# Kernel optimization log

Hardware: AMD Instinct MI355X
Metric: run time of the kernel (lower is better)

## Reference

```python
import jax, jax.numpy as jnp
import numpy as np

B, S, D, H = 4, 1024, 1024, 16
HD = D // H
EPS = 1e-5


def _layernorm(x, g, b):
    m = jnp.mean(x, axis=-1, keepdims=True)
    v = jnp.mean((x - m) ** 2, axis=-1, keepdims=True)
    return (x - m) * jax.lax.rsqrt(v + EPS) * g + b


def setup_inputs() -> dict:
    key = jax.random.key(0)
    ks = jax.random.split(key, 8)
    sc = 1.0 / np.sqrt(D)
    return {
        "x": jax.random.normal(ks[0], (B, S, D), dtype=jnp.float32),
        "seq_len": jax.random.randint(ks[1], (B,), 1, S + 1, dtype=jnp.int32),
        "Wq": jax.random.normal(ks[2], (D, D), dtype=jnp.float32) * sc,
        "bq": jnp.zeros((D,), dtype=jnp.float32),
        "Wk": jax.random.normal(ks[3], (D, D), dtype=jnp.float32) * sc,
        "bk": jnp.zeros((D,), dtype=jnp.float32),
        "Wv": jax.random.normal(ks[4], (D, D), dtype=jnp.float32) * sc,
        "bv": jnp.zeros((D,), dtype=jnp.float32),
        "ln_g": jnp.ones((HD,), dtype=jnp.float32),
        "ln_b": jnp.zeros((HD,), dtype=jnp.float32),
    }


def reference(x, seq_len, Wq, bq, Wk, bk, Wv, bv, ln_g, ln_b):
    # Faithful quirk: k and v are projections of the ALREADY projected q.
    q = x @ Wq.T + bq                      # [B,S,D]
    k = q @ Wk.T + bk
    v = q @ Wv.T + bv
    # [B,S,D] -> [B,H,S,HD]
    def split_heads(t):
        return t.reshape(B, S, H, HD).transpose(0, 2, 1, 3)
    q, k, v = split_heads(q), split_heads(k), split_heads(v)
    # shared per-head LayerNorm over head_dim
    q = _layernorm(q, ln_g, ln_b)
    k = _layernorm(k, ln_g, ln_b)
    v = _layernorm(v, ln_g, ln_b)
    # raw scores (no temperature scaling in the original; temperature=1.0 unused)
    scores = jnp.einsum("bhqd,bhkd->bhqk", q, k)
    # encoder_mask: multiplicative validity mask on key positions, repeated per head
    mask = (jnp.arange(S)[None, :] < seq_len[:, None]).astype(scores.dtype)  # [B,S]
    scores = scores * mask[:, None, None, :]
    attn = jax.nn.softmax(scores, axis=-1)
    # dropout is identity at inference
    out = jnp.einsum("bhqk,bhkd->bhqd", attn, v)
    return out.transpose(0, 2, 1, 3).reshape(B, S, D)
```

## Files before the change

### kernel.cpp

```cpp
#include <hip/hip_runtime.h>

#define B_  4
#define S_  1024
#define D_  1024
#define H_  16
#define HD_ 64
#define EPS_ 1e-5f

typedef _Float16 f16x8 __attribute__((ext_vector_type(8)));
typedef _Float16 f16x4 __attribute__((ext_vector_type(4)));
typedef __bf16 bf16x8 __attribute__((ext_vector_type(8)));
typedef float  f32x4  __attribute__((ext_vector_type(4)));
typedef unsigned short ushort4v __attribute__((ext_vector_type(4)));
typedef unsigned short ushort8v __attribute__((ext_vector_type(8)));

#define GLD16(gp, lp) __builtin_amdgcn_global_load_lds( \
    (const __attribute__((address_space(1))) void*)(gp), \
    (__attribute__((address_space(3))) void*)(lp), 16, 0, 0)

__global__ __launch_bounds__(256) void cvt_all(
    const float* __restrict__ x,  _Float16* __restrict__ xh,
    const float* __restrict__ Wq, _Float16* __restrict__ wqh,
    const float* __restrict__ Wk, _Float16* __restrict__ wkh,
    const float* __restrict__ Wv, _Float16* __restrict__ wvh,
    float* __restrict__ Vtail) {
  int bid = blockIdx.x;
  if (bid >= 7168) {
    int i = (bid - 7168) * 1024 + threadIdx.x * 4;
    *(float4*)(Vtail + i) = make_float4(0.f, 0.f, 0.f, 0.f);
    return;
  }
  const float* src; _Float16* dst; int base;
  if (bid < 4096)      { src = x;  dst = xh;  base = bid; }
  else if (bid < 5120) { src = Wq; dst = wqh; base = bid - 4096; }
  else if (bid < 6144) { src = Wk; dst = wkh; base = bid - 5120; }
  else                 { src = Wv; dst = wvh; base = bid - 6144; }
  int i = base * 1024 + threadIdx.x * 4;
  float4 f = *(const float4*)(src + i);
  f16x4 h;
  h.x = (_Float16)f.x; h.y = (_Float16)f.y; h.z = (_Float16)f.z; h.w = (_Float16)f.w;
  *(f16x4*)(dst + i) = h;
}

__global__ __launch_bounds__(256, 2) void gemm_q_ln(
    const _Float16* __restrict__ A,
    const _Float16* __restrict__ Bw,
    const float* __restrict__ bias,
    const float* __restrict__ ln_g, const float* __restrict__ ln_b,
    _Float16* __restrict__ qh,
    _Float16* __restrict__ Qn)
{
  __shared__ _Float16 As[2 * 128 * 32];
  __shared__ _Float16 Bs[2 * 64 * 32];

  int tid  = threadIdx.x;
  int lane = tid & 63;
  int wave = tid >> 6;
  int qd = lane >> 4, l15 = lane & 15;

  long row0 = (long)blockIdx.y * 128;
  long col0 = (long)blockIdx.x * 64;

  int r_a = tid >> 2;
  int c_a = (tid & 3) * 8;

  f32x4 acc[2][4] = {};

  for (int kk = 0; kk < D_; kk += 64) {
    GLD16(A  + (row0 + r_a) * D_ + kk + c_a,           As + tid * 8);
    GLD16(A  + (row0 + 64 + r_a) * D_ + kk + c_a,      As + 2048 + tid * 8);
    GLD16(A  + (row0 + r_a) * D_ + kk + 32 + c_a,      As + 4096 + tid * 8);
    GLD16(A  + (row0 + 64 + r_a) * D_ + kk + 32 + c_a, As + 6144 + tid * 8);
    GLD16(Bw + (col0 + r_a) * D_ + kk + c_a,           Bs + tid * 8);
    GLD16(Bw + (col0 + r_a) * D_ + kk + 32 + c_a,      Bs + 2048 + tid * 8);
    __syncthreads();

    for (int ks = 0; ks < 2; ks++) {
      f16x8 af[2], bfr[4];
      for (int i = 0; i < 2; i++)
        af[i]  = *(const f16x8*)(As + ks * 4096 + (wave * 32 + i * 16 + l15) * 32 + qd * 8);
      for (int j = 0; j < 4; j++)
        bfr[j] = *(const f16x8*)(Bs + ks * 2048 + (j * 16 + l15) * 32 + qd * 8);
      for (int i = 0; i < 2; i++)
        for (int j = 0; j < 4; j++)
          acc[i][j] = __builtin_amdgcn_mfma_f32_16x16x32_f16(af[i], bfr[j], acc[i][j], 0, 0, 0);
    }
    __syncthreads();
  }

  int h = blockIdx.x;
  long rw = row0 + wave * 32;
  int bb = (int)(rw >> 10);
  long bh = (long)bb * H_ + h;
  float gv[4], bl[4], bc[4];
  for (int j = 0; j < 4; j++) {
    int d = j * 16 + l15;
    gv[j] = ln_g[d]; bl[j] = ln_b[d]; bc[j] = bias[h * 64 + d];
  }
  for (int i = 0; i < 2; i++) {
    float m4[4], i4[4];
    for (int r = 0; r < 4; r++) {
      float s = 0.f, q = 0.f;
      for (int j = 0; j < 4; j++) {
        float y = acc[i][j][r] + bc[j];
        s += y; q = fmaf(y, y, q);
      }
      for (int off = 1; off < 16; off <<= 1) {
        s += __shfl_xor(s, off, 64);
        q += __shfl_xor(q, off, 64);
      }
      float m = s * (1.f / 64.f);
      m4[r] = m;
      i4[r] = rsqrtf(q * (1.f / 64.f) - m * m + EPS_);
    }
    for (int r = 0; r < 4; r++) {
      long srow = rw + i * 16 + qd * 4 + r;
      long sloc = srow & (S_ - 1);
      for (int j = 0; j < 4; j++) {
        float y = acc[i][j][r] + bc[j];
        qh[srow * D_ + h * 64 + j * 16 + l15] = (_Float16)y;
        Qn[(bh * S_ + sloc) * HD_ + j * 16 + l15] =
            (_Float16)((y - m4[r]) * i4[r] * gv[j] + bl[j]);
      }
    }
  }
}

__global__ __launch_bounds__(256, 2) void gemm_kv_ln(
    const _Float16* __restrict__ A,
    const _Float16* __restrict__ Bk, const float* __restrict__ bk,
    const _Float16* __restrict__ Bv, const float* __restrict__ bv,
    const float* __restrict__ ln_g, const float* __restrict__ ln_b,
    const int* __restrict__ seq_len,
    _Float16* __restrict__ Kn,
    unsigned short* __restrict__ Vt,
    float* __restrict__ Vtail)
{
  const _Float16* Bm = blockIdx.z ? Bv : Bk;
  const float* bias  = blockIdx.z ? bv : bk;

  __shared__ _Float16 As[2 * 128 * 32];
  __shared__ _Float16 Bs[2 * 128 * 32];

  int tid  = threadIdx.x;
  int lane = tid & 63;
  int wave = tid >> 6;
  int wm = wave >> 1, wn = wave & 1;
  int qd = lane >> 4, l15 = lane & 15;

  long row0 = (long)blockIdx.y * 128;
  long col0 = (long)blockIdx.x * 128;

  int r_a = tid >> 2;
  int c_a = (tid & 3) * 8;

  f32x4 acc[4][4] = {};

  for (int kk = 0; kk < D_; kk += 64) {
    GLD16(A  + (row0 + r_a) * D_ + kk + c_a,           As + tid * 8);
    GLD16(A  + (row0 + 64 + r_a) * D_ + kk + c_a,      As + 2048 + tid * 8);
    GLD16(A  + (row0 + r_a) * D_ + kk + 32 + c_a,      As + 4096 + tid * 8);
    GLD16(A  + (row0 + 64 + r_a) * D_ + kk + 32 + c_a, As + 6144 + tid * 8);
    GLD16(Bm + (col0 + r_a) * D_ + kk + c_a,           Bs + tid * 8);
    GLD16(Bm + (col0 + 64 + r_a) * D_ + kk + c_a,      Bs + 2048 + tid * 8);
    GLD16(Bm + (col0 + r_a) * D_ + kk + 32 + c_a,      Bs + 4096 + tid * 8);
    GLD16(Bm + (col0 + 64 + r_a) * D_ + kk + 32 + c_a, Bs + 6144 + tid * 8);
    __syncthreads();

    for (int ks = 0; ks < 2; ks++) {
      f16x8 af[4], bfr[4];
      for (int t = 0; t < 4; t++) {
        af[t]  = *(const f16x8*)(As + ks * 4096 + (wm * 64 + t * 16 + l15) * 32 + qd * 8);
        bfr[t] = *(const f16x8*)(Bs + ks * 4096 + (wn * 64 + t * 16 + l15) * 32 + qd * 8);
      }
      for (int i = 0; i < 4; i++)
        for (int j = 0; j < 4; j++)
          acc[i][j] = __builtin_amdgcn_mfma_f32_16x16x32_f16(af[i], bfr[j], acc[i][j], 0, 0, 0);
    }
    __syncthreads();
  }

  int h = blockIdx.x * 2 + wn;
  long rw = row0 + wm * 64;
  int bb = (int)(rw >> 10);
  long bh = (long)bb * H_ + h;
  float gv[4], bl[4], bc[4];
  for (int j = 0; j < 4; j++) {
    int d = j * 16 + l15;
    gv[j] = ln_g[d]; bl[j] = ln_b[d]; bc[j] = bias[h * 64 + d];
  }

  if (blockIdx.z == 0) {
    for (int i = 0; i < 4; i++) {
      float m4[4], i4[4];
      for (int r = 0; r < 4; r++) {
        float s = 0.f, q = 0.f;
        for (int j = 0; j < 4; j++) {
          float y = acc[i][j][r] + bc[j];
          s += y; q = fmaf(y, y, q);
        }
        for (int off = 1; off < 16; off <<= 1) {
          s += __shfl_xor(s, off, 64);
          q += __shfl_xor(q, off, 64);
        }
        float m = s * (1.f / 64.f);
        m4[r] = m;
        i4[r] = rsqrtf(q * (1.f / 64.f) - m * m + EPS_);
      }
      for (int r = 0; r < 4; r++) {
        long sloc = (rw + i * 16 + qd * 4 + r) & (S_ - 1);
        for (int j = 0; j < 4; j++) {
          float y = acc[i][j][r] + bc[j];
          Kn[(bh * S_ + sloc) * HD_ + j * 16 + l15] =
              (_Float16)((y - m4[r]) * i4[r] * gv[j] + bl[j]);
        }
      }
    }
  } else {
    int len = seq_len[bb];
    float tsum[4] = {0.f, 0.f, 0.f, 0.f};
    for (int i = 0; i < 4; i++) {
      float m4[4], i4[4];
      for (int r = 0; r < 4; r++) {
        float s = 0.f, q = 0.f;
        for (int j = 0; j < 4; j++) {
          float y = acc[i][j][r] + bc[j];
          s += y; q = fmaf(y, y, q);
        }
        for (int off = 1; off < 16; off <<= 1) {
          s += __shfl_xor(s, off, 64);
          q += __shfl_xor(q, off, 64);
        }
        float m = s * (1.f / 64.f);
        m4[r] = m;
        i4[r] = rsqrtf(q * (1.f / 64.f) - m * m + EPS_);
      }
      int s0loc = (int)((rw + i * 16 + qd * 4) & (S_ - 1));
      for (int j = 0; j < 4; j++) {
        ushort4v w;
        for (int r = 0; r < 4; r++) {
          float y = acc[i][j][r] + bc[j];
          float vo = (y - m4[r]) * i4[r] * gv[j] + bl[j];
          __bf16 vb = (__bf16)vo;
          union { __bf16 hh; unsigned short uu; } cv; cv.hh = vb;
          w[r] = cv.uu;
          if (s0loc + r >= len) tsum[j] += (float)vb;
        }
        *(ushort4v*)(Vt + (bh * HD_ + j * 16 + l15) * S_ + s0loc) = w;
      }
    }
    if (((int)(rw & (S_ - 1)) + 64) > len)
      for (int j = 0; j < 4; j++)
        atomicAdd(&Vtail[bh * HD_ + j * 16 + l15], tsum[j]);
  }
}

__global__ __launch_bounds__(256, 4) void attn(
    const _Float16* __restrict__ Qn,
    const _Float16* __restrict__ Kn,
    const unsigned short* __restrict__ Vt,
    const float* __restrict__ Vtail,
    const int* __restrict__ seq_len,
    float* __restrict__ out)
{
  __shared__ _Float16 Ks[2][64 * 32];
  __shared__ unsigned short Vts[2][64 * 32];
  __shared__ __bf16 Ps[4][16 * 72];

  int tid = threadIdx.x, lane = tid & 63, wave = tid >> 6;
  int qd = lane >> 4, l15 = lane & 15;
  int b = blockIdx.x;
  int h = blockIdx.y;
  int q0 = blockIdx.z * 64;
  long bh = (long)b * H_ + h;
  int len = seq_len[b];
  int ntile = (len + 63) >> 6;

  int skey = tid >> 2;
  int schunk = (tid & 3) * 8;

  f16x8 qf[2];
  {
    const _Float16* qp = Qn + (bh * S_ + q0 + wave * 16 + l15) * HD_;
    qf[0] = *(const f16x8*)(qp + qd * 8);
    qf[1] = *(const f16x8*)(qp + 32 + qd * 8);
  }
  float tv[4];
  for (int t = 0; t < 4; t++) tv[t] = Vtail[bh * HD_ + t * 16 + l15];

  f32x4 o[4] = {};
  float den[4] = {0.f, 0.f, 0.f, 0.f};

  for (int kt = 0; kt < ntile; kt++) {
    GLD16(Kn + (bh * S_ + kt * 64 + skey) * HD_ + schunk,      &Ks[0][0] + tid * 8);
    GLD16(Kn + (bh * S_ + kt * 64 + skey) * HD_ + 32 + schunk, &Ks[1][0] + tid * 8);
    GLD16(Vt + (bh * HD_ + skey) * S_ + kt * 64 + schunk,      &Vts[0][0] + tid * 8);
    GLD16(Vt + (bh * HD_ + skey) * S_ + kt * 64 + 32 + schunk, &Vts[1][0] + tid * 8);
    __syncthreads();

    f32x4 sacc[4] = {};
    for (int tn = 0; tn < 4; tn++) {
      f16x8 kf0 = *(const f16x8*)(&Ks[0][0] + (tn * 16 + l15) * 32 + qd * 8);
      f16x8 kf1 = *(const f16x8*)(&Ks[1][0] + (tn * 16 + l15) * 32 + qd * 8);
      sacc[tn] = __builtin_amdgcn_mfma_f32_16x16x32_f16(qf[0], kf0, sacc[tn], 0, 0, 0);
      sacc[tn] = __builtin_amdgcn_mfma_f32_16x16x32_f16(qf[1], kf1, sacc[tn], 0, 0, 0);
    }

    if (kt * 64 + 64 <= len) {
      for (int tn = 0; tn < 4; tn++)
        for (int r = 0; r < 4; r++) {
          float p = __expf(sacc[tn][r]);
          __bf16 pb = (__bf16)p;
          den[r] += (float)pb;
          Ps[wave][(qd * 4 + r) * 72 + tn * 16 + l15] = pb;
        }
    } else {
      for (int tn = 0; tn < 4; tn++) {
        int kg = kt * 64 + tn * 16 + l15;
        bool valid = kg < len;
        for (int r = 0; r < 4; r++) {
          float p = valid ? __expf(sacc[tn][r]) : 0.f;
          __bf16 pb = (__bf16)p;
          den[r] += (float)pb;
          Ps[wave][(qd * 4 + r) * 72 + tn * 16 + l15] = pb;
        }
      }
    }

    bf16x8 pf0 = *(const bf16x8*)(&Ps[wave][l15 * 72 + qd * 8]);
    bf16x8 pf1 = *(const bf16x8*)(&Ps[wave][l15 * 72 + 32 + qd * 8]);
    for (int t = 0; t < 4; t++) {
      bf16x8 vf0 = *(const bf16x8*)(&Vts[0][0] + (t * 16 + l15) * 32 + qd * 8);
      bf16x8 vf1 = *(const bf16x8*)(&Vts[1][0] + (t * 16 + l15) * 32 + qd * 8);
      o[t] = __builtin_amdgcn_mfma_f32_16x16x32_bf16(pf0, vf0, o[t], 0, 0, 0);
      o[t] = __builtin_amdgcn_mfma_f32_16x16x32_bf16(pf1, vf1, o[t], 0, 0, 0);
    }
    __syncthreads();
  }

  for (int t = 0; t < 4; t++)
    for (int r = 0; r < 4; r++) o[t][r] += tv[t];

  float tden = (float)(S_ - len);
  for (int r = 0; r < 4; r++) {
    for (int off = 1; off < 16; off <<= 1)
      den[r] += __shfl_xor(den[r], off, 64);
    den[r] += tden;
  }

  for (int t = 0; t < 4; t++)
    for (int r = 0; r < 4; r++) {
      long s = q0 + wave * 16 + qd * 4 + r;
      long dcol = (long)h * HD_ + t * 16 + l15;
      out[((long)b * S_ + s) * D_ + dcol] = o[t][r] / den[r];
    }
}

extern "C" void kernel_launch(void* const* d_in, const int* in_sizes, int n_in,
                              void* d_out, int out_size, void* d_ws, size_t ws_size,
                              hipStream_t stream) {
  const float* x     = (const float*)d_in[0];
  const int*  seq    = (const int*)d_in[1];
  const float* Wq    = (const float*)d_in[2];
  const float* bq    = (const float*)d_in[3];
  const float* Wk    = (const float*)d_in[4];
  const float* bk    = (const float*)d_in[5];
  const float* Wv    = (const float*)d_in[6];
  const float* bv    = (const float*)d_in[7];
  const float* ln_g  = (const float*)d_in[8];
  const float* ln_b  = (const float*)d_in[9];
  float* out = (float*)d_out;

  char* ws = (char*)d_ws;
  _Float16* xh  = (_Float16*)(ws);
  _Float16* wqh = (_Float16*)(ws + (8l  << 20));
  _Float16* wkh = (_Float16*)(ws + (10l << 20));
  _Float16* wvh = (_Float16*)(ws + (12l << 20));
  float*    Vtail = (float*)(ws + (14l << 20));
  _Float16* qh  = (_Float16*)(ws + (16l << 20));
  _Float16* Qn  = (_Float16*)(ws + (40l << 20));
  _Float16* Kn  = (_Float16*)(ws + (48l << 20));
  unsigned short* Vt = (unsigned short*)(ws + (56l << 20));

  cvt_all<<<7172, 256, 0, stream>>>(x, xh, Wq, wqh, Wk, wkh, Wv, wvh, Vtail);

  dim3 g1(D_ / 64, (B_ * S_) / 128);
  gemm_q_ln<<<g1, 256, 0, stream>>>(xh, wqh, bq, ln_g, ln_b, qh, Qn);

  dim3 g2(D_ / 128, (B_ * S_) / 128, 2);
  gemm_kv_ln<<<g2, 256, 0, stream>>>(qh, wkh, bk, wvh, bv, ln_g, ln_b, seq,
                                     Kn, Vt, Vtail);

  dim3 g4(B_, H_, S_ / 64);
  attn<<<g4, 256, 0, stream>>>(Qn, Kn, Vt, Vtail, seq, out);
}
```

Measured before the change: 168.6 us.

## Fold Wq into K/V weights so K and V project directly from x

```diff
diff --git a/kernel.cpp b/kernel.cpp
--- a/kernel.cpp
+++ b/kernel.cpp
@@ -12,7 +12,6 @@
 typedef __bf16 bf16x8 __attribute__((ext_vector_type(8)));
 typedef float  f32x4  __attribute__((ext_vector_type(4)));
 typedef unsigned short ushort4v __attribute__((ext_vector_type(4)));
-typedef unsigned short ushort8v __attribute__((ext_vector_type(8)));
 
 #define GLD16(gp, lp) __builtin_amdgcn_global_load_lds( \
     (const __attribute__((address_space(1))) void*)(gp), \
@@ -23,10 +22,32 @@
     const float* __restrict__ Wq, _Float16* __restrict__ wqh,
     const float* __restrict__ Wk, _Float16* __restrict__ wkh,
     const float* __restrict__ Wv, _Float16* __restrict__ wvh,
+    _Float16* __restrict__ wqT,
     float* __restrict__ Vtail) {
+  __shared__ _Float16 tl[64][72];
   int bid = blockIdx.x;
+  int tid = threadIdx.x;
+  if (bid >= 7172) {
+    int tb = bid - 7172;
+    int r0 = (tb >> 4) * 64, c0 = (tb & 15) * 64;
+    int r = tid >> 2, cq = (tid & 3) * 16;
+    for (int u = 0; u < 16; u += 4) {
+      float4 f = *(const float4*)(Wq + (long)(r0 + r) * D_ + c0 + cq + u);
+      tl[r][cq + u + 0] = (_Float16)f.x;
+      tl[r][cq + u + 1] = (_Float16)f.y;
+      tl[r][cq + u + 2] = (_Float16)f.z;
+      tl[r][cq + u + 3] = (_Float16)f.w;
+    }
+    __syncthreads();
+    f16x8 o0, o1;
+    for (int u = 0; u < 8; u++) o0[u] = tl[cq + u][r];
+    for (int u = 0; u < 8; u++) o1[u] = tl[cq + 8 + u][r];
+    *(f16x8*)(wqT + (long)(c0 + r) * D_ + r0 + cq) = o0;
+    *(f16x8*)(wqT + (long)(c0 + r) * D_ + r0 + cq + 8) = o1;
+    return;
+  }
   if (bid >= 7168) {
-    int i = (bid - 7168) * 1024 + threadIdx.x * 4;
+    int i = (bid - 7168) * 1024 + tid * 4;
     *(float4*)(Vtail + i) = make_float4(0.f, 0.f, 0.f, 0.f);
     return;
   }
@@ -35,32 +56,67 @@
   else if (bid < 5120) { src = Wq; dst = wqh; base = bid - 4096; }
   else if (bid < 6144) { src = Wk; dst = wkh; base = bid - 5120; }
   else                 { src = Wv; dst = wvh; base = bid - 6144; }
-  int i = base * 1024 + threadIdx.x * 4;
+  int i = base * 1024 + tid * 4;
   float4 f = *(const float4*)(src + i);
   f16x4 h;
   h.x = (_Float16)f.x; h.y = (_Float16)f.y; h.z = (_Float16)f.z; h.w = (_Float16)f.w;
   *(f16x4*)(dst + i) = h;
 }
 
-__global__ __launch_bounds__(256, 2) void gemm_q_ln(
-    const _Float16* __restrict__ A,
-    const _Float16* __restrict__ Bw,
-    const float* __restrict__ bias,
+__global__ __launch_bounds__(256, 2) void proj_q_comb(
+    const _Float16* __restrict__ xh,
+    const _Float16* __restrict__ wqh,
+    const _Float16* __restrict__ wkh,
+    const _Float16* __restrict__ wvh,
+    const _Float16* __restrict__ wqT,
+    const float* __restrict__ Wkf, const float* __restrict__ Wvf,
+    const float* __restrict__ bq,  const float* __restrict__ bk,
+    const float* __restrict__ bv,
     const float* __restrict__ ln_g, const float* __restrict__ ln_b,
-    _Float16* __restrict__ qh,
-    _Float16* __restrict__ Qn)
+    _Float16* __restrict__ Qn,
+    _Float16* __restrict__ wkqh, _Float16* __restrict__ wvqh,
+    float* __restrict__ bkc, float* __restrict__ bvc)
 {
   __shared__ _Float16 As[2 * 128 * 32];
   __shared__ _Float16 Bs[2 * 64 * 32];
 
-  int tid  = threadIdx.x;
+  int bid = blockIdx.x;
+  int tid = threadIdx.x;
+
+  if (bid >= 768) {
+    int bb = bid - 768;
+    int rib = tid >> 4, L = tid & 15;
+    int ro = bb * 16 + rib;
+    int z = ro >> 10, oo = ro & 1023;
+    const float* W    = z ? Wvf : Wkf;
+    const float* bsrc = z ? bv  : bk;
+    float* dst        = z ? bvc : bkc;
+    float s = 0.f;
+    for (int t = 0; t < 64; t++)
+      s += W[(long)oo * D_ + t * 16 + L] * bq[t * 16 + L];
+    for (int off = 1; off < 16; off <<= 1)
+      s += __shfl_xor(s, off, 16);
+    if (L == 0) dst[oo] = s + bsrc[oo];
+    return;
+  }
+
+  bool isq = bid < 512;
+  const _Float16 *A, *Bw;
+  _Float16* Cw = nullptr;
+  int bx, by;
+  if (isq) { A = xh; Bw = wqh; bx = bid & 15; by = bid >> 4; }
+  else {
+    int cb = bid - 512;
+    int z = cb >> 7, cc = cb & 127;
+    bx = cc & 15; by = cc >> 4;
+    A = z ? wvh : wkh; Bw = wqT; Cw = z ? wvqh : wkqh;
+  }
+
   int lane = tid & 63;
   int wave = tid >> 6;
   int qd = lane >> 4, l15 = lane & 15;
-
-  long row0 = (long)blockIdx.y * 128;
-  long col0 = (long)blockIdx.x * 64;
-
+  long row0 = (long)by * 128;
+  long col0 = (long)bx * 64;
   int r_a = tid >> 2;
   int c_a = (tid & 3) * 8;
 
@@ -88,6 +144,104 @@
     __syncthreads();
   }
 
+  if (!isq) {
+    for (int i = 0; i < 2; i++)
+      for (int r = 0; r < 4; r++) {
+        long row = row0 + wave * 32 + i * 16 + qd * 4 + r;
+        for (int j = 0; j < 4; j++)
+          Cw[row * D_ + col0 + j * 16 + l15] = (_Float16)acc[i][j][r];
+      }
+    return;
+  }
+
+  int h = bx;
+  long rw = row0 + wave * 32;
+  int bb2 = (int)(rw >> 10);
+  long bh = (long)bb2 * H_ + h;
+  float gv[4], bl[4], bc[4];
+  for (int j = 0; j < 4; j++) {
+    int d = j * 16 + l15;
+    gv[j] = ln_g[d]; bl[j] = ln_b[d]; bc[j] = bq[h * 64 + d];
+  }
+  for (int i = 0; i < 2; i++) {
+    float m4[4], i4[4];
+    for (int r = 0; r < 4; r++) {
+      float s = 0.f, q = 0.f;
+      for (int j = 0; j < 4; j++) {
+        float y = acc[i][j][r] + bc[j];
+        s += y; q = fmaf(y, y, q);
+      }
+      for (int off = 1; off < 16; off <<= 1) {
+        s += __shfl_xor(s, off, 64);
+        q += __shfl_xor(q, off, 64);
+      }
+      float m = s * (1.f / 64.f);
+      m4[r] = m;
+      i4[r] = rsqrtf(q * (1.f / 64.f) - m * m + EPS_);
+    }
+    for (int r = 0; r < 4; r++) {
+      long sloc = (rw + i * 16 + qd * 4 + r) & (S_ - 1);
+      for (int j = 0; j < 4; j++) {
+        float y = acc[i][j][r] + bc[j];
+        Qn[(bh * S_ + sloc) * HD_ + j * 16 + l15] =
+            (_Float16)((y - m4[r]) * i4[r] * gv[j] + bl[j]);
+      }
+    }
+  }
+}
+
+__global__ __launch_bounds__(256, 2) void proj_kv(
+    const _Float16* __restrict__ xh,
+    const _Float16* __restrict__ wkqh, const float* __restrict__ bkc,
+    const _Float16* __restrict__ wvqh, const float* __restrict__ bvc,
+    const float* __restrict__ ln_g, const float* __restrict__ ln_b,
+    const int* __restrict__ seq_len,
+    _Float16* __restrict__ Kn,
+    unsigned short* __restrict__ Vt,
+    float* __restrict__ Vtail)
+{
+  int z = blockIdx.z;
+  const _Float16* Bw = z ? wvqh : wkqh;
+  const float* bias  = z ? bvc : bkc;
+
+  __shared__ _Float16 As[2 * 128 * 32];
+  __shared__ _Float16 Bs[2 * 64 * 32];
+
+  int tid  = threadIdx.x;
+  int lane = tid & 63;
+  int wave = tid >> 6;
+  int qd = lane >> 4, l15 = lane & 15;
+
+  long row0 = (long)blockIdx.y * 128;
+  long col0 = (long)blockIdx.x * 64;
+
+  int r_a = tid >> 2;
+  int c_a = (tid & 3) * 8;
+
+  f32x4 acc[2][4] = {};
+
+  for (int kk = 0; kk < D_; kk += 64) {
+    GLD16(xh + (row0 + r_a) * D_ + kk + c_a,           As + tid * 8);
+    GLD16(xh + (row0 + 64 + r_a) * D_ + kk + c_a,      As + 2048 + tid * 8);
+    GLD16(xh + (row0 + r_a) * D_ + kk + 32 + c_a,      As + 4096 + tid * 8);
+    GLD16(xh + (row0 + 64 + r_a) * D_ + kk + 32 + c_a, As + 6144 + tid * 8);
+    GLD16(Bw + (col0 + r_a) * D_ + kk + c_a,           Bs + tid * 8);
+    GLD16(Bw + (col0 + r_a) * D_ + kk + 32 + c_a,      Bs + 2048 + tid * 8);
+    __syncthreads();
+
+    for (int ks = 0; ks < 2; ks++) {
+      f16x8 af[2], bfr[4];
+      for (int i = 0; i < 2; i++)
+        af[i]  = *(const f16x8*)(As + ks * 4096 + (wave * 32 + i * 16 + l15) * 32 + qd * 8);
+      for (int j = 0; j < 4; j++)
+        bfr[j] = *(const f16x8*)(Bs + ks * 2048 + (j * 16 + l15) * 32 + qd * 8);
+      for (int i = 0; i < 2; i++)
+        for (int j = 0; j < 4; j++)
+          acc[i][j] = __builtin_amdgcn_mfma_f32_16x16x32_f16(af[i], bfr[j], acc[i][j], 0, 0, 0);
+    }
+    __syncthreads();
+  }
+
   int h = blockIdx.x;
   long rw = row0 + wave * 32;
   int bb = (int)(rw >> 10);
@@ -97,101 +251,9 @@
     int d = j * 16 + l15;
     gv[j] = ln_g[d]; bl[j] = ln_b[d]; bc[j] = bias[h * 64 + d];
   }
-  for (int i = 0; i < 2; i++) {
-    float m4[4], i4[4];
-    for (int r = 0; r < 4; r++) {
-      float s = 0.f, q = 0.f;
-      for (int j = 0; j < 4; j++) {
-        float y = acc[i][j][r] + bc[j];
-        s += y; q = fmaf(y, y, q);
-      }
-      for (int off = 1; off < 16; off <<= 1) {
-        s += __shfl_xor(s, off, 64);
-        q += __shfl_xor(q, off, 64);
-      }
-      float m = s * (1.f / 64.f);
-      m4[r] = m;
-      i4[r] = rsqrtf(q * (1.f / 64.f) - m * m + EPS_);
-    }
-    for (int r = 0; r < 4; r++) {
-      long srow = rw + i * 16 + qd * 4 + r;
-      long sloc = srow & (S_ - 1);
-      for (int j = 0; j < 4; j++) {
-        float y = acc[i][j][r] + bc[j];
-        qh[srow * D_ + h * 64 + j * 16 + l15] = (_Float16)y;
-        Qn[(bh * S_ + sloc) * HD_ + j * 16 + l15] =
-            (_Float16)((y - m4[r]) * i4[r] * gv[j] + bl[j]);
-      }
-    }
-  }
-}
-
-__global__ __launch_bounds__(256, 2) void gemm_kv_ln(
-    const _Float16* __restrict__ A,
-    const _Float16* __restrict__ Bk, const float* __restrict__ bk,
-    const _Float16* __restrict__ Bv, const float* __restrict__ bv,
-    const float* __restrict__ ln_g, const float* __restrict__ ln_b,
-    const int* __restrict__ seq_len,
-    _Float16* __restrict__ Kn,
-    unsigned short* __restrict__ Vt,
-    float* __restrict__ Vtail)
-{
-  const _Float16* Bm = blockIdx.z ? Bv : Bk;
-  const float* bias  = blockIdx.z ? bv : bk;
-
-  __shared__ _Float16 As[2 * 128 * 32];
-  __shared__ _Float16 Bs[2 * 128 * 32];
-
-  int tid  = threadIdx.x;
-  int lane = tid & 63;
-  int wave = tid >> 6;
-  int wm = wave >> 1, wn = wave & 1;
-  int qd = lane >> 4, l15 = lane & 15;
-
-  long row0 = (long)blockIdx.y * 128;
-  long col0 = (long)blockIdx.x * 128;
-
-  int r_a = tid >> 2;
-  int c_a = (tid & 3) * 8;
-
-  f32x4 acc[4][4] = {};
-
-  for (int kk = 0; kk < D_; kk += 64) {
-    GLD16(A  + (row0 + r_a) * D_ + kk + c_a,           As + tid * 8);
-    GLD16(A  + (row0 + 64 + r_a) * D_ + kk + c_a,      As + 2048 + tid * 8);
-    GLD16(A  + (row0 + r_a) * D_ + kk + 32 + c_a,      As + 4096 + tid * 8);
-    GLD16(A  + (row0 + 64 + r_a) * D_ + kk + 32 + c_a, As + 6144 + tid * 8);
-    GLD16(Bm + (col0 + r_a) * D_ + kk + c_a,           Bs + tid * 8);
-    GLD16(Bm + (col0 + 64 + r_a) * D_ + kk + c_a,      Bs + 2048 + tid * 8);
-    GLD16(Bm + (col0 + r_a) * D_ + kk + 32 + c_a,      Bs + 4096 + tid * 8);
-    GLD16(Bm + (col0 + 64 + r_a) * D_ + kk + 32 + c_a, Bs + 6144 + tid * 8);
-    __syncthreads();
-
-    for (int ks = 0; ks < 2; ks++) {
-      f16x8 af[4], bfr[4];
-      for (int t = 0; t < 4; t++) {
-        af[t]  = *(const f16x8*)(As + ks * 4096 + (wm * 64 + t * 16 + l15) * 32 + qd * 8);
-        bfr[t] = *(const f16x8*)(Bs + ks * 4096 + (wn * 64 + t * 16 + l15) * 32 + qd * 8);
-      }
-      for (int i = 0; i < 4; i++)
-        for (int j = 0; j < 4; j++)
-          acc[i][j] = __builtin_amdgcn_mfma_f32_16x16x32_f16(af[i], bfr[j], acc[i][j], 0, 0, 0);
-    }
-    __syncthreads();
-  }
-
-  int h = blockIdx.x * 2 + wn;
-  long rw = row0 + wm * 64;
-  int bb = (int)(rw >> 10);
-  long bh = (long)bb * H_ + h;
-  float gv[4], bl[4], bc[4];
-  for (int j = 0; j < 4; j++) {
-    int d = j * 16 + l15;
-    gv[j] = ln_g[d]; bl[j] = ln_b[d]; bc[j] = bias[h * 64 + d];
-  }
-
-  if (blockIdx.z == 0) {
-    for (int i = 0; i < 4; i++) {
+
+  if (z == 0) {
+    for (int i = 0; i < 2; i++) {
       float m4[4], i4[4];
       for (int r = 0; r < 4; r++) {
         float s = 0.f, q = 0.f;
@@ -219,7 +281,7 @@
   } else {
     int len = seq_len[bb];
     float tsum[4] = {0.f, 0.f, 0.f, 0.f};
-    for (int i = 0; i < 4; i++) {
+    for (int i = 0; i < 2; i++) {
       float m4[4], i4[4];
       for (int r = 0; r < 4; r++) {
         float s = 0.f, q = 0.f;
@@ -249,7 +311,7 @@
         *(ushort4v*)(Vt + (bh * HD_ + j * 16 + l15) * S_ + s0loc) = w;
       }
     }
-    if (((int)(rw & (S_ - 1)) + 64) > len)
+    if (((int)(rw & (S_ - 1)) + 32) > len)
       for (int j = 0; j < 4; j++)
         atomicAdd(&Vtail[bh * HD_ + j * 16 + l15], tsum[j]);
   }
@@ -372,24 +434,29 @@
   float* out = (float*)d_out;
 
   char* ws = (char*)d_ws;
-  _Float16* xh  = (_Float16*)(ws);
-  _Float16* wqh = (_Float16*)(ws + (8l  << 20));
-  _Float16* wkh = (_Float16*)(ws + (10l << 20));
-  _Float16* wvh = (_Float16*)(ws + (12l << 20));
-  float*    Vtail = (float*)(ws + (14l << 20));
-  _Float16* qh  = (_Float16*)(ws + (16l << 20));
-  _Float16* Qn  = (_Float16*)(ws + (40l << 20));
-  _Float16* Kn  = (_Float16*)(ws + (48l << 20));
-  unsigned short* Vt = (unsigned short*)(ws + (56l << 20));
-
-  cvt_all<<<7172, 256, 0, stream>>>(x, xh, Wq, wqh, Wk, wkh, Wv, wvh, Vtail);
-
-  dim3 g1(D_ / 64, (B_ * S_) / 128);
-  gemm_q_ln<<<g1, 256, 0, stream>>>(xh, wqh, bq, ln_g, ln_b, qh, Qn);
-
-  dim3 g2(D_ / 128, (B_ * S_) / 128, 2);
-  gemm_kv_ln<<<g2, 256, 0, stream>>>(qh, wkh, bk, wvh, bv, ln_g, ln_b, seq,
-                                     Kn, Vt, Vtail);
+  _Float16* xh   = (_Float16*)(ws);
+  _Float16* wqh  = (_Float16*)(ws + (8l  << 20));
+  _Float16* wkh  = (_Float16*)(ws + (10l << 20));
+  _Float16* wvh  = (_Float16*)(ws + (12l << 20));
+  float*    Vtail= (float*)(ws + (14l << 20));
+  _Float16* wqTh = (_Float16*)(ws + (15l << 20));
+  _Float16* wkqh = (_Float16*)(ws + (17l << 20));
+  _Float16* wvqh = (_Float16*)(ws + (19l << 20));
+  float*    bkc  = (float*)(ws + (21l << 20));
+  float*    bvc  = (float*)(ws + (21l << 20) + 4096);
+  _Float16* Qn   = (_Float16*)(ws + (24l << 20));
+  _Float16* Kn   = (_Float16*)(ws + (32l << 20));
+  unsigned short* Vt = (unsigned short*)(ws + (40l << 20));
+
+  cvt_all<<<7428, 256, 0, stream>>>(x, xh, Wq, wqh, Wk, wkh, Wv, wvh, wqTh, Vtail);
+
+  proj_q_comb<<<896, 256, 0, stream>>>(xh, wqh, wkh, wvh, wqTh, Wk, Wv,
+                                       bq, bk, bv, ln_g, ln_b,
+                                       Qn, wkqh, wvqh, bkc, bvc);
+
+  dim3 g2(D_ / 64, (B_ * S_) / 128, 2);
+  proj_kv<<<g2, 256, 0, stream>>>(xh, wkqh, bkc, wvqh, bvc, ln_g, ln_b, seq,
+                                  Kn, Vt, Vtail);
 
   dim3 g4(B_, H_, S_ / 64);
   attn<<<g4, 256, 0, stream>>>(Qn, Kn, Vt, Vtail, seq, out);
```

Measured after the change: 187.7 us. +11.3%, slower.
